# Optimization experiments

Measured on AMD Instinct MI355X. Metric: run time of the kernel, lower is better.

The kernel has to match this reference:

```python
import jax, jax.numpy as jnp
import numpy as np

B, N, D = 32, 1024, 256  # batch, nodes, feature dim (input=hidden=output=256)


def setup_inputs() -> dict:
    key = jax.random.key(0)
    ks = jax.random.split(key, 9)
    x = jax.random.normal(ks[0], (B, N, D), dtype=jnp.float32)
    # binary node mask (multiplied in, so float dtype)
    mask = (jax.random.uniform(ks[1], (B, N)) > 0.2).astype(jnp.float32)
    # dense nonneg adjacency; row sums > 0 almost surely
    adj = jax.random.uniform(ks[2], (B, N, N), dtype=jnp.float32)
    s = 1.0 / np.sqrt(D)
    W0 = jax.random.normal(ks[3], (D, D), dtype=jnp.float32) * s
    b0 = jnp.zeros((D,), dtype=jnp.float32)
    W1 = jax.random.normal(ks[4], (D, D), dtype=jnp.float32) * s
    b1 = jnp.zeros((D,), dtype=jnp.float32)
    W2 = jax.random.normal(ks[5], (D, D), dtype=jnp.float32) * s
    b2 = jnp.zeros((D,), dtype=jnp.float32)
    return {"x": x, "mask": mask, "adj": adj,
            "W0": W0, "b0": b0, "W1": W1, "b1": b1, "W2": W2, "b2": b2}


def reference(x, mask, adj, W0, b0, W1, b1, W2, b2):
    # D_hat = diag(1/rowsum(adj)) with inf -> 0; diag matmul == row-wise scale
    deg = jnp.sum(adj, axis=-1)                                   # [B,N]
    dinv = jnp.where(deg != 0, 1.0 / jnp.where(deg != 0, deg, 1.0), 0.0)
    adj_n = adj * dinv[..., None]                                 # [B,N,N]
    xm = mask[..., None]                                          # [B,N,1]
    # dropout is identity in eval mode
    for W, b in ((W0, b0), (W1, b1), (W2, b2)):
        x = jnp.matmul(x, W.T) + b                                # linear
        x = jnp.einsum('bnm,bmd->bnd', adj_n, x)                  # aggregate
        x = x * xm                                                # mask
        x = jax.nn.gelu(x, approximate=False)                     # exact gelu (torch F.gelu)
    return x
```

## Files before the change

### kernel.cpp

```cpp
#include <hip/hip_runtime.h>
#include <stdint.h>


typedef __attribute__((ext_vector_type(8))) short short8;
typedef __attribute__((ext_vector_type(4))) float f32x4;

__device__ __forceinline__ uint16_t f2bf(float f) {
  uint32_t u = __float_as_uint(f);
  u += 0x7FFF + ((u >> 16) & 1);
  return (uint16_t)(u >> 16);
}
__device__ __forceinline__ float bf2f(uint16_t h) {
  return __uint_as_float(((uint32_t)h) << 16);
}
__device__ __forceinline__ float gelu_exact(float v) {
  return 0.5f * v * (1.0f + erff(v * 0.70710678118654752f));
}
__device__ __forceinline__ f32x4 mfma16(short8 a, short8 b, f32x4 c) {
  return __builtin_amdgcn_mfma_f32_16x16x32_bf16(a, b, c, 0, 0, 0);
}

#define GLD16(gsrc, ldst) __builtin_amdgcn_global_load_lds(                    \
    (const __attribute__((address_space(1))) void*)(gsrc),                     \
    (__attribute__((address_space(3))) void*)(ldst), 16, 0, 0)

__global__ void k_split(const float* __restrict__ src, uint16_t* __restrict__ h,
                        uint16_t* __restrict__ l, int n4) {
  int i = blockIdx.x * blockDim.x + threadIdx.x;
  if (i >= n4) return;
  const float4 v = ((const float4*)src)[i];
  float vv[4] = {v.x, v.y, v.z, v.w};
  ushort4 hh, ll;
  uint16_t* hp = (uint16_t*)&hh;
  uint16_t* lp = (uint16_t*)&ll;
#pragma unroll
  for (int e = 0; e < 4; ++e) {
    uint16_t hb = f2bf(vv[e]);
    hp[e] = hb;
    lp[e] = f2bf(vv[e] - bf2f(hb));
  }
  ((ushort4*)h)[i] = hh;
  ((ushort4*)l)[i] = ll;
}

__global__ void k_norm_adj(const float* __restrict__ adj, uint16_t* __restrict__ An) {
  const int r = blockIdx.x;
  const int t = threadIdx.x;
  const float* row = adj + (size_t)r * 1024;
  const float4 v = *(const float4*)(row + t * 4);
  float s = v.x + v.y + v.z + v.w;
#pragma unroll
  for (int off = 32; off; off >>= 1) s += __shfl_down(s, off);
  __shared__ float ws[4];
  if ((t & 63) == 0) ws[t >> 6] = s;
  __syncthreads();
  const float deg = ws[0] + ws[1] + ws[2] + ws[3];
  const float dinv = (deg != 0.f) ? 1.f / deg : 0.f;
  ushort4 o;
  uint16_t* op = (uint16_t*)&o;
  float vv[4] = {v.x, v.y, v.z, v.w};
#pragma unroll
  for (int e = 0; e < 4; ++e) op[e] = f2bf(vv[e] * dinv);
  const int b = r >> 10, node = r & 1023;
  const int mb = node >> 7, rr = node & 127;
  const int kt = t >> 3, ko = (t * 4) & 31;
  const size_t oo = (size_t)(b * 8 + mb) * 131072 + kt * 4096 + rr * 32 + ko;
  *(ushort4*)(An + oo) = o;
}

__global__ __launch_bounds__(256) void k_linear(
    const uint16_t* __restrict__ Xh, const uint16_t* __restrict__ Xl,
    const uint16_t* __restrict__ Wh, const uint16_t* __restrict__ Wl,
    const float* __restrict__ bias,
    uint16_t* __restrict__ Yth) {
  __shared__ __align__(16) uint8_t smem[32768];
  const int tid = threadIdx.x;
  const int lane = tid & 63;
  const int wave = tid >> 6;
  const int wr = wave >> 1, wc = wave & 1;
  const int m0 = blockIdx.x * 128;
  const int n0 = blockIdx.y * 128;
  const int lm = lane & 15, g = lane >> 4;
  const int srow = lane >> 2;
  const int skof = (lane & 3) * 8;

  f32x4 acc[4][4] = {};

  for (int kt = 0; kt < 8; ++kt) {
    const int k0 = kt * 32;
    __syncthreads();
#pragma unroll
    for (int j = 0; j < 8; ++j) {
      const int c = j * 4 + wave;
      const int sub = c & 7, which = c >> 3;
      const int row = sub * 16 + srow;
      const uint16_t* src;
      if (which == 0)      src = Xh + (size_t)(m0 + row) * 256 + k0 + skof;
      else if (which == 1) src = Xl + (size_t)(m0 + row) * 256 + k0 + skof;
      else if (which == 2) src = Wh + (size_t)(n0 + row) * 256 + k0 + skof;
      else                 src = Wl + (size_t)(n0 + row) * 256 + k0 + skof;
      GLD16(src, smem + c * 1024);
    }
    asm volatile("s_waitcnt vmcnt(0)" ::: "memory");
    __syncthreads();

    const uint8_t* Ahs = smem;
    const uint8_t* Als = smem + 8192;
    const uint8_t* Bhs = smem + 16384;
    const uint8_t* Bls = smem + 24576;
    short8 ah[4], al[4], bh[4], bl[4];
#pragma unroll
    for (int f = 0; f < 4; ++f) {
      ah[f] = *(const short8*)(Ahs + (wr * 64 + f * 16 + lm) * 64 + g * 16);
      al[f] = *(const short8*)(Als + (wr * 64 + f * 16 + lm) * 64 + g * 16);
      bh[f] = *(const short8*)(Bhs + (wc * 64 + f * 16 + lm) * 64 + g * 16);
      bl[f] = *(const short8*)(Bls + (wc * 64 + f * 16 + lm) * 64 + g * 16);
    }
#pragma unroll
    for (int fm = 0; fm < 4; ++fm)
#pragma unroll
      for (int fn = 0; fn < 4; ++fn) {
        acc[fm][fn] = mfma16(ah[fm], bh[fn], acc[fm][fn]);
        acc[fm][fn] = mfma16(ah[fm], bl[fn], acc[fm][fn]);
        acc[fm][fn] = mfma16(al[fm], bh[fn], acc[fm][fn]);
      }
  }

#pragma unroll
  for (int fn = 0; fn < 4; ++fn) {
    const int n = n0 + wc * 64 + fn * 16 + lm;
    const float bv = bias[n];
#pragma unroll
    for (int fm = 0; fm < 4; ++fm) {
      const int mg = m0 + wr * 64 + fm * 16 + g * 4;
      const int bb = mg >> 10, node = mg & 1023;
      const int kt = node >> 5, ko = node & 31;
      ushort4 hh;
      uint16_t* hp = (uint16_t*)&hh;
#pragma unroll
      for (int e = 0; e < 4; ++e) hp[e] = f2bf(acc[fm][fn][e] + bv);
      const size_t o = ((size_t)(bb * 32 + kt) * 256 + n) * 32 + ko;
      *(ushort4*)(Yth + o) = hh;
    }
  }
}

#define STAGE(T, SSL) {                                                        \
    _Pragma("unroll")                                                          \
    for (int j = 0; j < 4; ++j) {                                              \
      const int c = w * 4 + j;                                                 \
      const uint16_t* src = (c < 8)                                            \
          ? aStep + (size_t)(T) * 4096 + c * 512                               \
          : yStep + (size_t)(T) * 8192 + (c - 8) * 512;                        \
      GLD16(src, smem + (SSL) + c * 1024);                                     \
    }                                                                          \
  }

template <bool LAST>
__global__ __launch_bounds__(256, 2) void k_agg(
    const uint16_t* __restrict__ An,
    const uint16_t* __restrict__ Yth,
    const float* __restrict__ mask,
    uint16_t* __restrict__ Xh, uint16_t* __restrict__ Xl,
    float* __restrict__ out) {
  __shared__ __align__(16) uint8_t smem[49152];
  const int tid = threadIdx.x;
  const int lane = tid & 63;
  const int w = tid >> 6;
  const int wm = w >> 1, wn = w & 1;
  const int id = blockIdx.x;
  const int swz = (id & 7) * 64 + (id >> 3);
  const int b = swz >> 4;
  const int rest = swz & 15;
  const int mb = rest >> 1;
  const int nh = rest & 1;
  const int lm = lane & 15, g = lane >> 4;

  const uint16_t* aStep = An + (size_t)(b * 8 + mb) * 131072 + lane * 8;
  const uint16_t* yStep = Yth + (size_t)b * 262144 + nh * 4096 + lane * 8;

  const int aoff = (wm * 64 + lm) * 64 + g * 16;
  const int boff = 8192 + (wn * 64 + lm) * 64 + g * 16;

  f32x4 acc[4][4] = {};

  STAGE(0, 0);
  STAGE(1, 16384);

  int csl = 0, ssl = 32768;
#pragma unroll 1
  for (int t = 0; t < 32; ++t) {
    if (t < 31) { asm volatile("s_waitcnt vmcnt(4)" ::: "memory"); }
    else        { asm volatile("s_waitcnt vmcnt(0)" ::: "memory"); }
    __builtin_amdgcn_s_barrier();
    __builtin_amdgcn_sched_barrier(0);
    if (t < 30) { STAGE(t + 2, ssl); }
    __builtin_amdgcn_sched_barrier(0);

    const uint8_t* sb = smem + csl;
    short8 af[4];
#pragma unroll
    for (int f = 0; f < 4; ++f) af[f] = *(const short8*)(sb + aoff + f * 1024);
    __builtin_amdgcn_s_setprio(1);
#pragma unroll
    for (int fn = 0; fn < 4; ++fn) {
      const short8 hf = *(const short8*)(sb + boff + fn * 1024);
#pragma unroll
      for (int fm = 0; fm < 4; ++fm)
        acc[fm][fn] = mfma16(af[fm], hf, acc[fm][fn]);
    }
    __builtin_amdgcn_s_setprio(0);

    csl += 16384; if (csl == 49152) csl = 0;
    ssl += 16384; if (ssl == 49152) ssl = 0;
  }

  const float* mk_b = mask + b * 1024;
#pragma unroll
  for (int fm = 0; fm < 4; ++fm) {
    const int m = mb * 128 + wm * 64 + fm * 16 + g * 4;
    float mk[4];
#pragma unroll
    for (int e = 0; e < 4; ++e) mk[e] = mk_b[m + e];
#pragma unroll
    for (int fn = 0; fn < 4; ++fn) {
      const int n = nh * 128 + wn * 64 + fn * 16 + lm;
#pragma unroll
      for (int e = 0; e < 4; ++e) {
        const float v = gelu_exact(acc[fm][fn][e] * mk[e]);
        const size_t o = ((size_t)(b * 1024 + m + e)) * 256 + n;
        if (LAST) {
          out[o] = v;
        } else {
          const uint16_t hb = f2bf(v);
          Xh[o] = hb;
          Xl[o] = f2bf(v - bf2f(hb));
        }
      }
    }
  }
}

extern "C" void kernel_launch(void* const* d_in, const int* in_sizes, int n_in,
                              void* d_out, int out_size, void* d_ws, size_t ws_size,
                              hipStream_t stream) {
  const float* x    = (const float*)d_in[0];
  const float* mask = (const float*)d_in[1];
  const float* adj  = (const float*)d_in[2];
  const float* W[3]  = {(const float*)d_in[3], (const float*)d_in[5], (const float*)d_in[7]};
  const float* bs[3] = {(const float*)d_in[4], (const float*)d_in[6], (const float*)d_in[8]};

  uint8_t* ws = (uint8_t*)d_ws;
  uint16_t* An  = (uint16_t*)(ws);
  uint16_t* Xh  = (uint16_t*)(ws + 67108864);
  uint16_t* Xl  = (uint16_t*)(ws + 83886080);
  uint16_t* Yth = (uint16_t*)(ws + 100663296);
  uint16_t* Wh  = (uint16_t*)(ws + 134217728);
  uint16_t* Wl  = (uint16_t*)(ws + 134610944);

  k_split<<<dim3(8192), 256, 0, stream>>>(x, Xh, Xl, 2097152);
  for (int i = 0; i < 3; ++i)
    k_split<<<dim3(64), 256, 0, stream>>>(W[i], Wh + i * 65536, Wl + i * 65536, 16384);
  k_norm_adj<<<dim3(32768), 256, 0, stream>>>(adj, An);

  for (int l = 0; l < 3; ++l) {
    k_linear<<<dim3(256, 2), 256, 0, stream>>>(Xh, Xl, Wh + l * 65536, Wl + l * 65536,
                                               bs[l], Yth);
    if (l < 2)
      k_agg<false><<<dim3(512), 256, 0, stream>>>(An, Yth, mask, Xh, Xl, nullptr);
    else
      k_agg<true><<<dim3(512), 256, 0, stream>>>(An, Yth, mask, nullptr, nullptr,
                                                 (float*)d_out);
  }
}
```

Measured before the change: 200.5 us.

## Drop low-order activation split and deepen aggregation pipeline to four stages

Activations are now held as a single bf16 value instead of a hi/lo bf16 pair. This removes the Xl buffer, one third of the MFMAs and A-tile loads in the linear kernel, and half of the bf16 stores in the aggregation epilogue. The weights keep their hi/lo split. Separately, the aggregation kernel's shared-memory ring grows from three to four 16KB stages, prefetching three tiles ahead with adjusted vmcnt waits. The cost is lower activation precision, and the larger LDS footprint may reduce how many blocks fit per CU.

Result: faster. 184.7 us (-7.9%).

```diff
diff --git a/kernel.cpp b/kernel.cpp
--- a/kernel.cpp
+++ b/kernel.cpp
@@ -23,6 +23,19 @@
 #define GLD16(gsrc, ldst) __builtin_amdgcn_global_load_lds(                    \
     (const __attribute__((address_space(1))) void*)(gsrc),                     \
     (__attribute__((address_space(3))) void*)(ldst), 16, 0, 0)
+
+__global__ void k_cast(const float* __restrict__ src, uint16_t* __restrict__ h,
+                       int n4) {
+  int i = blockIdx.x * blockDim.x + threadIdx.x;
+  if (i >= n4) return;
+  const float4 v = ((const float4*)src)[i];
+  float vv[4] = {v.x, v.y, v.z, v.w};
+  ushort4 hh;
+  uint16_t* hp = (uint16_t*)&hh;
+#pragma unroll
+  for (int e = 0; e < 4; ++e) hp[e] = f2bf(vv[e]);
+  ((ushort4*)h)[i] = hh;
+}
 
 __global__ void k_split(const float* __restrict__ src, uint16_t* __restrict__ h,
                         uint16_t* __restrict__ l, int n4) {
@@ -69,11 +82,11 @@
 }
 
 __global__ __launch_bounds__(256) void k_linear(
-    const uint16_t* __restrict__ Xh, const uint16_t* __restrict__ Xl,
+    const uint16_t* __restrict__ Xh,
     const uint16_t* __restrict__ Wh, const uint16_t* __restrict__ Wl,
     const float* __restrict__ bias,
     uint16_t* __restrict__ Yth) {
-  __shared__ __align__(16) uint8_t smem[32768];
+  __shared__ __align__(16) uint8_t smem[24576];
   const int tid = threadIdx.x;
   const int lane = tid & 63;
   const int wave = tid >> 6;
@@ -90,14 +103,13 @@
     const int k0 = kt * 32;
     __syncthreads();
 #pragma unroll
-    for (int j = 0; j < 8; ++j) {
+    for (int j = 0; j < 6; ++j) {
       const int c = j * 4 + wave;
       const int sub = c & 7, which = c >> 3;
       const int row = sub * 16 + srow;
       const uint16_t* src;
       if (which == 0)      src = Xh + (size_t)(m0 + row) * 256 + k0 + skof;
-      else if (which == 1) src = Xl + (size_t)(m0 + row) * 256 + k0 + skof;
-      else if (which == 2) src = Wh + (size_t)(n0 + row) * 256 + k0 + skof;
+      else if (which == 1) src = Wh + (size_t)(n0 + row) * 256 + k0 + skof;
       else                 src = Wl + (size_t)(n0 + row) * 256 + k0 + skof;
       GLD16(src, smem + c * 1024);
     }
@@ -105,14 +117,12 @@
     __syncthreads();
 
     const uint8_t* Ahs = smem;
-    const uint8_t* Als = smem + 8192;
-    const uint8_t* Bhs = smem + 16384;
-    const uint8_t* Bls = smem + 24576;
-    short8 ah[4], al[4], bh[4], bl[4];
+    const uint8_t* Bhs = smem + 8192;
+    const uint8_t* Bls = smem + 16384;
+    short8 ah[4], bh[4], bl[4];
 #pragma unroll
     for (int f = 0; f < 4; ++f) {
       ah[f] = *(const short8*)(Ahs + (wr * 64 + f * 16 + lm) * 64 + g * 16);
-      al[f] = *(const short8*)(Als + (wr * 64 + f * 16 + lm) * 64 + g * 16);
       bh[f] = *(const short8*)(Bhs + (wc * 64 + f * 16 + lm) * 64 + g * 16);
       bl[f] = *(const short8*)(Bls + (wc * 64 + f * 16 + lm) * 64 + g * 16);
     }
@@ -122,7 +132,6 @@
       for (int fn = 0; fn < 4; ++fn) {
         acc[fm][fn] = mfma16(ah[fm], bh[fn], acc[fm][fn]);
         acc[fm][fn] = mfma16(ah[fm], bl[fn], acc[fm][fn]);
-        acc[fm][fn] = mfma16(al[fm], bh[fn], acc[fm][fn]);
       }
   }
 
@@ -161,9 +170,9 @@
     const uint16_t* __restrict__ An,
     const uint16_t* __restrict__ Yth,
     const float* __restrict__ mask,
-    uint16_t* __restrict__ Xh, uint16_t* __restrict__ Xl,
+    uint16_t* __restrict__ Xh,
     float* __restrict__ out) {
-  __shared__ __align__(16) uint8_t smem[49152];
+  __shared__ __align__(16) uint8_t smem[65536];
   const int tid = threadIdx.x;
   const int lane = tid & 63;
   const int w = tid >> 6;
@@ -186,15 +195,17 @@
 
   STAGE(0, 0);
   STAGE(1, 16384);
-
-  int csl = 0, ssl = 32768;
+  STAGE(2, 32768);
+
+  int csl = 0, ssl = 49152;
 #pragma unroll 1
   for (int t = 0; t < 32; ++t) {
-    if (t < 31) { asm volatile("s_waitcnt vmcnt(4)" ::: "memory"); }
-    else        { asm volatile("s_waitcnt vmcnt(0)" ::: "memory"); }
+    if (t < 30)      { asm volatile("s_waitcnt vmcnt(8)" ::: "memory"); }
+    else if (t == 30){ asm volatile("s_waitcnt vmcnt(4)" ::: "memory"); }
+    else             { asm volatile("s_waitcnt vmcnt(0)" ::: "memory"); }
     __builtin_amdgcn_s_barrier();
     __builtin_amdgcn_sched_barrier(0);
-    if (t < 30) { STAGE(t + 2, ssl); }
+    if (t < 29) { STAGE(t + 3, ssl); }
     __builtin_amdgcn_sched_barrier(0);
 
     const uint8_t* sb = smem + csl;
@@ -211,8 +222,8 @@
     }
     __builtin_amdgcn_s_setprio(0);
 
-    csl += 16384; if (csl == 49152) csl = 0;
-    ssl += 16384; if (ssl == 49152) ssl = 0;
+    csl += 16384; if (csl == 65536) csl = 0;
+    ssl += 16384; if (ssl == 65536) ssl = 0;
   }
 
   const float* mk_b = mask + b * 1024;
@@ -232,9 +243,7 @@
         if (LAST) {
           out[o] = v;
         } else {
-          const uint16_t hb = f2bf(v);
-          Xh[o] = hb;
-          Xl[o] = f2bf(v - bf2f(hb));
+          Xh[o] = f2bf(v);
         }
       }
     }
@@ -253,23 +262,22 @@
   uint8_t* ws = (uint8_t*)d_ws;
   uint16_t* An  = (uint16_t*)(ws);
   uint16_t* Xh  = (uint16_t*)(ws + 67108864);
-  uint16_t* Xl  = (uint16_t*)(ws + 83886080);
-  uint16_t* Yth = (uint16_t*)(ws + 100663296);
-  uint16_t* Wh  = (uint16_t*)(ws + 134217728);
-  uint16_t* Wl  = (uint16_t*)(ws + 134610944);
-
-  k_split<<<dim3(8192), 256, 0, stream>>>(x, Xh, Xl, 2097152);
+  uint16_t* Yth = (uint16_t*)(ws + 83886080);
+  uint16_t* Wh  = (uint16_t*)(ws + 100663296);
+  uint16_t* Wl  = (uint16_t*)(ws + 101056512);
+
+  k_cast<<<dim3(8192), 256, 0, stream>>>(x, Xh, 2097152);
   for (int i = 0; i < 3; ++i)
     k_split<<<dim3(64), 256, 0, stream>>>(W[i], Wh + i * 65536, Wl + i * 65536, 16384);
   k_norm_adj<<<dim3(32768), 256, 0, stream>>>(adj, An);
 
   for (int l = 0; l < 3; ++l) {
-    k_linear<<<dim3(256, 2), 256, 0, stream>>>(Xh, Xl, Wh + l * 65536, Wl + l * 65536,
+    k_linear<<<dim3(256, 2), 256, 0, stream>>>(Xh, Wh + l * 65536, Wl + l * 65536,
                                                bs[l], Yth);
     if (l < 2)
-      k_agg<false><<<dim3(512), 256, 0, stream>>>(An, Yth, mask, Xh, Xl, nullptr);
+      k_agg<false><<<dim3(512), 256, 0, stream>>>(An, Yth, mask, Xh, nullptr);
     else
-      k_agg<true><<<dim3(512), 256, 0, stream>>>(An, Yth, mask, nullptr, nullptr,
+      k_agg<true><<<dim3(512), 256, 0, stream>>>(An, Yth, mask, nullptr,
                                                  (float*)d_out);
   }
 }
```
